# Kernel optimization log

Measured on AMD Instinct MI355X. Metric: run time of the kernel, lower is better.

Reference implementation:

```python
import jax, jax.numpy as jnp
import numpy as np

B, C, H, W = 4, 64, 64, 64
CQK = C // 8


def setup_inputs() -> dict:
    key = jax.random.key(0)
    k0, k1, k2, k3, k4 = jax.random.split(key, 5)
    x = jax.random.normal(k0, (B, C, H, W), dtype=jnp.float32)
    # Conv1d kernel_size=1, bias=False -> plain [out, in] matmul weights
    Wq = jax.random.normal(k1, (CQK, C), dtype=jnp.float32) * 0.05
    Wk = jax.random.normal(k2, (CQK, C), dtype=jnp.float32) * 0.05
    Wv = jax.random.normal(k3, (C, C), dtype=jnp.float32) * 0.05
    # torch init is 0; use a nonzero scalar so the attention path is exercised
    gamma = jax.random.uniform(k4, (1,), dtype=jnp.float32)
    return {"x": x, "Wq": Wq, "Wk": Wk, "Wv": Wv, "gamma": gamma}


def reference(x, Wq, Wk, Wv, gamma):
    shape = x.shape                      # [B, C, H, W]
    xf = x.reshape(shape[0], shape[1], -1)  # [B, C, N]
    q = jnp.einsum('oc,bcn->bon', Wq, xf)   # [B, C/8, N]
    k = jnp.einsum('oc,bcn->bon', Wk, xf)   # [B, C/8, N]
    v = jnp.einsum('oc,bcn->bon', Wv, xf)   # [B, C, N]
    # score[b, n, m] = sum_c q[b, c, n] * k[b, c, m]  (no 1/sqrt(d) scale)
    score = jnp.einsum('bcn,bcm->bnm', q, k)  # [B, N, N]
    # unconventional softmax over dim=1 (rows/first N axis, i.e. per-column)
    score = jax.nn.softmax(score, axis=1)
    out = jnp.einsum('bcn,bnm->bcm', v, score)  # [B, C, N]
    attention = gamma * out + xf
    return attention.reshape(shape)
```

## Files before the change

kernel.cpp:

```cpp
#include <hip/hip_runtime.h>

#define BB 4
#define NN 4096

typedef __attribute__((ext_vector_type(8))) short short8v;
typedef __attribute__((ext_vector_type(4))) short short4v;
typedef __attribute__((ext_vector_type(4))) float float4v;
typedef __attribute__((ext_vector_type(16))) float f32x16;

__device__ __forceinline__ unsigned short f2bf_rn(float f) {
    unsigned u = __float_as_uint(f);
    u += 0x7FFFu + ((u >> 16) & 1u);
    return (unsigned short)(u >> 16);
}

__global__ __launch_bounds__(256) void qkv_kernel(
    const float* __restrict__ x,
    const float* __restrict__ Wq, const float* __restrict__ Wk,
    const float* __restrict__ Wv,
    unsigned short* __restrict__ Qt, unsigned short* __restrict__ Kt,
    unsigned short* __restrict__ Vsw)
{
    __shared__ __align__(16) unsigned short xs[64][68];
    __shared__ __align__(16) unsigned short Ot[64][72];

    const int t    = threadIdx.x;
    const int w    = t >> 6;
    const int lane = t & 63;
    const int quad = lane >> 4;
    const int l15  = lane & 15;
    const int b    = blockIdx.y;
    const int n0   = blockIdx.x * 64;

    #pragma unroll
    for (int i = 0; i < 4; ++i) {
        int c  = (t >> 4) + i * 16;
        int n4 = (t & 15) * 4;
        float4 xv = *(const float4*)&x[(size_t)(b * 64 + c) * NN + n0 + n4];
        short4v pk;
        pk[0] = (short)f2bf_rn(xv.x); pk[1] = (short)f2bf_rn(xv.y);
        pk[2] = (short)f2bf_rn(xv.z); pk[3] = (short)f2bf_rn(xv.w);
        *(short4v*)&xs[c][n4] = pk;
    }

    short8v bw[5][2];
    #pragma unroll
    for (int ot = 0; ot < 5; ++ot) {
        int o = ot * 16 + l15;
        const float* base = (o < 8)  ? (Wq + o * 64)
                           : (o < 16) ? (Wk + (o - 8) * 64)
                                      : (Wv + (o - 16) * 64);
        const float scale = (o < 8) ? 1.4426950408889634f : 1.0f;
        #pragma unroll
        for (int h = 0; h < 2; ++h) {
            float4 u0 = *(const float4*)&base[h * 32 + quad * 8];
            float4 u1 = *(const float4*)&base[h * 32 + quad * 8 + 4];
            short8v f;
            f[0] = (short)f2bf_rn(u0.x * scale); f[1] = (short)f2bf_rn(u0.y * scale);
            f[2] = (short)f2bf_rn(u0.z * scale); f[3] = (short)f2bf_rn(u0.w * scale);
            f[4] = (short)f2bf_rn(u1.x * scale); f[5] = (short)f2bf_rn(u1.y * scale);
            f[6] = (short)f2bf_rn(u1.z * scale); f[7] = (short)f2bf_rn(u1.w * scale);
            bw[ot][h] = f;
        }
    }
    __syncthreads();

    short8v a0, a1;
    {
        unsigned short* p0 = (unsigned short*)&a0;
        unsigned short* p1 = (unsigned short*)&a1;
        const int nn = w * 16 + l15;
        #pragma unroll
        for (int j = 0; j < 8; ++j) {
            p0[j] = xs[quad * 8 + j][nn];
            p1[j] = xs[32 + quad * 8 + j][nn];
        }
    }

    const float4v zacc = {0.f, 0.f, 0.f, 0.f};
    #pragma unroll
    for (int ot = 0; ot < 5; ++ot) {
        float4v d = __builtin_amdgcn_mfma_f32_16x16x32_bf16(a0, bw[ot][0], zacc, 0, 0, 0);
        d = __builtin_amdgcn_mfma_f32_16x16x32_bf16(a1, bw[ot][1], d, 0, 0, 0);
        if (ot == 0) {
            #pragma unroll
            for (int r = 0; r < 4; ++r) {
                unsigned short v = f2bf_rn(d[r]);
                size_t n = (size_t)(n0 + w * 16 + quad * 4 + r);
                if (l15 < 8) Qt[((size_t)b * NN + n) * 8 + l15] = v;
                else         Kt[((size_t)b * NN + n) * 8 + (l15 - 8)] = v;
            }
        } else {
            short4v pk;
            #pragma unroll
            for (int r = 0; r < 4; ++r) pk[r] = (short)f2bf_rn(d[r]);
            *(short4v*)&Ot[(ot - 1) * 16 + l15][w * 16 + quad * 4] = pk;
        }
    }
    __syncthreads();

    #pragma unroll
    for (int h = 0; h < 2; ++h) {
        int ci  = w * 2 + h;
        int ct  = ci >> 2, nsl = ci & 3;
        short8v d = *(const short8v*)&Ot[ct * 32 + (lane & 31)][nsl * 16 + ((lane >> 5) << 3)];
        size_t ns = (size_t)blockIdx.x * 4 + nsl;
        unsigned short* cb = Vsw + (((size_t)b * 2 + ct) * 256 + ns) * 512;
        *(short8v*)(cb + lane * 8) = d;
    }
}

__global__ __launch_bounds__(512, 4) void attn_kernel(
    const unsigned short* __restrict__ Qt,
    const unsigned short* __restrict__ Kt,
    const unsigned short* __restrict__ Vsw,
    const float* __restrict__ x, const float* __restrict__ gamma,
    float* __restrict__ out)
{
    __shared__ __align__(16) float Ored[4][64][36];
    __shared__ __align__(16) float Lred[8][32];
    __shared__ __align__(16) float Lf[32];

    const int t    = threadIdx.x;
    const int w    = t >> 6;
    const int lane = t & 63;
    const int hi   = lane >> 5;
    const int l31  = lane & 31;
    const int b    = blockIdx.y;
    const int m0   = blockIdx.x * 32;

    const short8v zfrag = {0, 0, 0, 0, 0, 0, 0, 0};
    const f32x16 zero16 = {0.f, 0.f, 0.f, 0.f, 0.f, 0.f, 0.f, 0.f,
                           0.f, 0.f, 0.f, 0.f, 0.f, 0.f, 0.f, 0.f};

    short8v bk = zfrag;
    if (!hi) bk = *(const short8v*)(Kt + ((size_t)b * NN + m0 + l31) * 8);

    f32x16 acc0 = zero16, acc1 = zero16;
    float La = 0.f, Lb = 0.f;

    const unsigned short* qp  = Qt + ((size_t)b * NN + w * 512) * 8;
    const unsigned short* v0p = Vsw + ((size_t)b * 2 * 256 + w * 32) * 512 + lane * 8;
    const unsigned short* v1p = v0p + 256 * 512;

    short8v aqn = zfrag;
    if (!hi) aqn = *(const short8v*)(qp + (size_t)l31 * 8);

    for (int it = 0; it < 16; ++it) {
        short8v a00 = *(const short8v*)(v0p + it * 1024);
        short8v a01 = *(const short8v*)(v0p + it * 1024 + 512);
        short8v a10 = *(const short8v*)(v1p + it * 1024);
        short8v a11 = *(const short8v*)(v1p + it * 1024 + 512);

        short8v aq = aqn;

        f32x16 s = __builtin_amdgcn_mfma_f32_32x32x16_bf16(aq, bk, zero16, 0, 0, 0);

        const int itn = (it + 1) & 15;
        if (!hi) aqn = *(const short8v*)(qp + (size_t)(itn * 32 + l31) * 8);

        unsigned xw[8];
        #pragma unroll
        for (int j = 0; j < 8; ++j) {
            float e0 = __builtin_amdgcn_exp2f(s[2 * j]);
            float e1 = __builtin_amdgcn_exp2f(s[2 * j + 1]);
            La += e0;
            Lb += e1;
            asm("v_cvt_pk_bf16_f32 %0, %1, %2" : "=v"(xw[j]) : "v"(e0), "v"(e1));
        }

        asm("v_permlane32_swap_b32 %0, %1" : "+v"(xw[2]), "+v"(xw[0]));
        asm("v_permlane32_swap_b32 %0, %1" : "+v"(xw[3]), "+v"(xw[1]));
        asm("v_permlane32_swap_b32 %0, %1" : "+v"(xw[6]), "+v"(xw[4]));
        asm("v_permlane32_swap_b32 %0, %1" : "+v"(xw[7]), "+v"(xw[5]));

        union { unsigned u[4]; short8v v; } bp0, bp1;
        bp0.u[0] = xw[0]; bp0.u[1] = xw[1]; bp0.u[2] = xw[2]; bp0.u[3] = xw[3];
        bp1.u[0] = xw[4]; bp1.u[1] = xw[5]; bp1.u[2] = xw[6]; bp1.u[3] = xw[7];

        __builtin_amdgcn_s_setprio(1);
        acc0 = __builtin_amdgcn_mfma_f32_32x32x16_bf16(a00, bp0.v, acc0, 0, 0, 0);
        acc0 = __builtin_amdgcn_mfma_f32_32x32x16_bf16(a01, bp1.v, acc0, 0, 0, 0);
        acc1 = __builtin_amdgcn_mfma_f32_32x32x16_bf16(a10, bp0.v, acc1, 0, 0, 0);
        acc1 = __builtin_amdgcn_mfma_f32_32x32x16_bf16(a11, bp1.v, acc1, 0, 0, 0);
        __builtin_amdgcn_s_setprio(0);
    }

    float Lacc = La + Lb;

    Lacc += __shfl_xor(Lacc, 32, 64);
    if (lane < 32) Lred[w][l31] = Lacc;

    if (w < 4) {
        #pragma unroll
        for (int r = 0; r < 16; ++r) {
            int c = (r & 3) + 8 * (r >> 2) + 4 * hi;
            Ored[w][c][l31]      = acc0[r];
            Ored[w][c + 32][l31] = acc1[r];
        }
    }
    __syncthreads();
    if (w >= 4) {
        #pragma unroll
        for (int r = 0; r < 16; ++r) {
            int c = (r & 3) + 8 * (r >> 2) + 4 * hi;
            Ored[w - 4][c][l31]      += acc0[r];
            Ored[w - 4][c + 32][l31] += acc1[r];
        }
    }
    if (t < 32) {
        float sum = Lred[0][t] + Lred[1][t] + Lred[2][t] + Lred[3][t]
                  + Lred[4][t] + Lred[5][t] + Lred[6][t] + Lred[7][t];
        Lf[t] = 1.f / sum;
    }
    __syncthreads();

    {
        const float gv = gamma[0];
        int c = t >> 3, m4 = (t & 7) * 4;
        float4 o = {0.f, 0.f, 0.f, 0.f};
        #pragma unroll
        for (int k2 = 0; k2 < 4; ++k2) {
            float4 v = *(const float4*)&Ored[k2][c][m4];
            o.x += v.x; o.y += v.y; o.z += v.z; o.w += v.w;
        }
        float4 lf = *(const float4*)&Lf[m4];
        size_t gbase = ((size_t)b * 64 + c) * NN + m0 + m4;
        float4 xv = *(const float4*)&x[gbase];
        float4 r;
        r.x = gv * o.x * lf.x + xv.x;
        r.y = gv * o.y * lf.y + xv.y;
        r.z = gv * o.z * lf.z + xv.z;
        r.w = gv * o.w * lf.w + xv.w;
        *(float4*)&out[gbase] = r;
    }
}

extern "C" void kernel_launch(void* const* d_in, const int* in_sizes, int n_in,
                              void* d_out, int out_size, void* d_ws, size_t ws_size,
                              hipStream_t stream) {
    const float* x     = (const float*)d_in[0];
    const float* Wq    = (const float*)d_in[1];
    const float* Wk    = (const float*)d_in[2];
    const float* Wv    = (const float*)d_in[3];
    const float* gamma = (const float*)d_in[4];
    float* out = (float*)d_out;

    unsigned short* ws = (unsigned short*)d_ws;
    unsigned short* Qt  = ws;
    unsigned short* Kt  = Qt + (size_t)BB * NN * 8;
    unsigned short* Vsw = Kt + (size_t)BB * NN * 8;

    qkv_kernel<<<dim3(NN / 64, BB), 256, 0, stream>>>(x, Wq, Wk, Wv, Qt, Kt, Vsw);
    attn_kernel<<<dim3(NN / 32, BB), 512, 0, stream>>>(Qt, Kt, Vsw, x, gamma, out);
}
```

Baseline: 85.07 us.

## Split qkv projection into finer blocks and compute softmax denominators with MFMA

The projection kernel now handles 32 positions per block with 512 threads, so there are twice as many blocks and each wave computes only one or two output tiles instead of five. The attention kernel drops the per-element VALU accumulation of exponentials and instead gets the column sums from two extra MFMAs against an all-ones bf16 operand. This offloads adds from the VALU, which is already busy with exp and packing, to the matrix unit. The cost is extra MFMA work per iteration, and the denominators are now summed from bf16-rounded exponentials.

Result: no change. 85.80 us (+0.9%).

```diff
diff --git a/kernel.cpp b/kernel.cpp
--- a/kernel.cpp
+++ b/kernel.cpp
@@ -14,79 +14,85 @@
     return (unsigned short)(u >> 16);
 }
 
-__global__ __launch_bounds__(256) void qkv_kernel(
+__global__ __launch_bounds__(512) void qkv_kernel(
     const float* __restrict__ x,
     const float* __restrict__ Wq, const float* __restrict__ Wk,
     const float* __restrict__ Wv,
     unsigned short* __restrict__ Qt, unsigned short* __restrict__ Kt,
     unsigned short* __restrict__ Vsw)
 {
-    __shared__ __align__(16) unsigned short xs[64][68];
-    __shared__ __align__(16) unsigned short Ot[64][72];
+    __shared__ __align__(16) unsigned short xs[64][40];
+    __shared__ __align__(16) unsigned short Ot[64][40];
 
     const int t    = threadIdx.x;
     const int w    = t >> 6;
     const int lane = t & 63;
     const int quad = lane >> 4;
     const int l15  = lane & 15;
+    const int hi   = lane >> 5;
+    const int l31  = lane & 31;
     const int b    = blockIdx.y;
-    const int n0   = blockIdx.x * 64;
-
-    #pragma unroll
-    for (int i = 0; i < 4; ++i) {
-        int c  = (t >> 4) + i * 16;
-        int n4 = (t & 15) * 4;
+    const int n0   = blockIdx.x * 32;
+
+    const float4v zacc4 = {0.f, 0.f, 0.f, 0.f};
+
+    {
+        int c = t >> 3, n4 = (t & 7) * 4;
         float4 xv = *(const float4*)&x[(size_t)(b * 64 + c) * NN + n0 + n4];
         short4v pk;
         pk[0] = (short)f2bf_rn(xv.x); pk[1] = (short)f2bf_rn(xv.y);
         pk[2] = (short)f2bf_rn(xv.z); pk[3] = (short)f2bf_rn(xv.w);
         *(short4v*)&xs[c][n4] = pk;
     }
-
-    short8v bw[5][2];
+    __syncthreads();
+
     #pragma unroll
-    for (int ot = 0; ot < 5; ++ot) {
+    for (int ti = 0; ti < 2; ++ti) {
+        int ot, nt;
+        if (ti == 0) { ot = w >> 1; nt = w & 1; }
+        else         { if (w >= 2) break; ot = 4; nt = w; }
+
         int o = ot * 16 + l15;
         const float* base = (o < 8)  ? (Wq + o * 64)
                            : (o < 16) ? (Wk + (o - 8) * 64)
                                       : (Wv + (o - 16) * 64);
         const float scale = (o < 8) ? 1.4426950408889634f : 1.0f;
-        #pragma unroll
-        for (int h = 0; h < 2; ++h) {
-            float4 u0 = *(const float4*)&base[h * 32 + quad * 8];
-            float4 u1 = *(const float4*)&base[h * 32 + quad * 8 + 4];
-            short8v f;
-            f[0] = (short)f2bf_rn(u0.x * scale); f[1] = (short)f2bf_rn(u0.y * scale);
-            f[2] = (short)f2bf_rn(u0.z * scale); f[3] = (short)f2bf_rn(u0.w * scale);
-            f[4] = (short)f2bf_rn(u1.x * scale); f[5] = (short)f2bf_rn(u1.y * scale);
-            f[6] = (short)f2bf_rn(u1.z * scale); f[7] = (short)f2bf_rn(u1.w * scale);
-            bw[ot][h] = f;
-        }
-    }
-    __syncthreads();
-
-    short8v a0, a1;
-    {
-        unsigned short* p0 = (unsigned short*)&a0;
-        unsigned short* p1 = (unsigned short*)&a1;
-        const int nn = w * 16 + l15;
-        #pragma unroll
-        for (int j = 0; j < 8; ++j) {
-            p0[j] = xs[quad * 8 + j][nn];
-            p1[j] = xs[32 + quad * 8 + j][nn];
-        }
-    }
-
-    const float4v zacc = {0.f, 0.f, 0.f, 0.f};
-    #pragma unroll
-    for (int ot = 0; ot < 5; ++ot) {
-        float4v d = __builtin_amdgcn_mfma_f32_16x16x32_bf16(a0, bw[ot][0], zacc, 0, 0, 0);
-        d = __builtin_amdgcn_mfma_f32_16x16x32_bf16(a1, bw[ot][1], d, 0, 0, 0);
+        short8v bw0, bw1;
+        {
+            float4 u0 = *(const float4*)&base[quad * 8];
+            float4 u1 = *(const float4*)&base[quad * 8 + 4];
+            bw0[0] = (short)f2bf_rn(u0.x * scale); bw0[1] = (short)f2bf_rn(u0.y * scale);
+            bw0[2] = (short)f2bf_rn(u0.z * scale); bw0[3] = (short)f2bf_rn(u0.w * scale);
+            bw0[4] = (short)f2bf_rn(u1.x * scale); bw0[5] = (short)f2bf_rn(u1.y * scale);
+            bw0[6] = (short)f2bf_rn(u1.z * scale); bw0[7] = (short)f2bf_rn(u1.w * scale);
+            float4 u2 = *(const float4*)&base[32 + quad * 8];
+            float4 u3 = *(const float4*)&base[32 + quad * 8 + 4];
+            bw1[0] = (short)f2bf_rn(u2.x * scale); bw1[1] = (short)f2bf_rn(u2.y * scale);
+            bw1[2] = (short)f2bf_rn(u2.z * scale); bw1[3] = (short)f2bf_rn(u2.w * scale);
+            bw1[4] = (short)f2bf_rn(u3.x * scale); bw1[5] = (short)f2bf_rn(u3.y * scale);
+            bw1[6] = (short)f2bf_rn(u3.z * scale); bw1[7] = (short)f2bf_rn(u3.w * scale);
+        }
+
+        short8v a0, a1;
+        {
+            unsigned short* p0 = (unsigned short*)&a0;
+            unsigned short* p1 = (unsigned short*)&a1;
+            const int nn = nt * 16 + l15;
+            #pragma unroll
+            for (int j = 0; j < 8; ++j) {
+                p0[j] = xs[quad * 8 + j][nn];
+                p1[j] = xs[32 + quad * 8 + j][nn];
+            }
+        }
+
+        float4v d = __builtin_amdgcn_mfma_f32_16x16x32_bf16(a0, bw0, zacc4, 0, 0, 0);
+        d = __builtin_amdgcn_mfma_f32_16x16x32_bf16(a1, bw1, d, 0, 0, 0);
+
         if (ot == 0) {
             #pragma unroll
             for (int r = 0; r < 4; ++r) {
                 unsigned short v = f2bf_rn(d[r]);
-                size_t n = (size_t)(n0 + w * 16 + quad * 4 + r);
+                size_t n = (size_t)(n0 + nt * 16 + quad * 4 + r);
                 if (l15 < 8) Qt[((size_t)b * NN + n) * 8 + l15] = v;
                 else         Kt[((size_t)b * NN + n) * 8 + (l15 - 8)] = v;
             }
@@ -94,17 +100,15 @@
             short4v pk;
             #pragma unroll
             for (int r = 0; r < 4; ++r) pk[r] = (short)f2bf_rn(d[r]);
-            *(short4v*)&Ot[(ot - 1) * 16 + l15][w * 16 + quad * 4] = pk;
-        }
-    }
-    __syncthreads();
-
-    #pragma unroll
-    for (int h = 0; h < 2; ++h) {
-        int ci  = w * 2 + h;
-        int ct  = ci >> 2, nsl = ci & 3;
-        short8v d = *(const short8v*)&Ot[ct * 32 + (lane & 31)][nsl * 16 + ((lane >> 5) << 3)];
-        size_t ns = (size_t)blockIdx.x * 4 + nsl;
+            *(short4v*)&Ot[(ot - 1) * 16 + l15][nt * 16 + quad * 4] = pk;
+        }
+    }
+    __syncthreads();
+
+    if (w < 4) {
+        int ct = w >> 1, nsl = w & 1;
+        short8v d = *(const short8v*)&Ot[ct * 32 + l31][nsl * 16 + hi * 8];
+        size_t ns = (size_t)blockIdx.x * 2 + nsl;
         unsigned short* cb = Vsw + (((size_t)b * 2 + ct) * 256 + ns) * 512;
         *(short8v*)(cb + lane * 8) = d;
     }
@@ -130,14 +134,15 @@
     const int m0   = blockIdx.x * 32;
 
     const short8v zfrag = {0, 0, 0, 0, 0, 0, 0, 0};
+    const short8v aones = {16256, 16256, 16256, 16256,
+                           16256, 16256, 16256, 16256};
     const f32x16 zero16 = {0.f, 0.f, 0.f, 0.f, 0.f, 0.f, 0.f, 0.f,
                            0.f, 0.f, 0.f, 0.f, 0.f, 0.f, 0.f, 0.f};
 
     short8v bk = zfrag;
     if (!hi) bk = *(const short8v*)(Kt + ((size_t)b * NN + m0 + l31) * 8);
 
-    f32x16 acc0 = zero16, acc1 = zero16;
-    float La = 0.f, Lb = 0.f;
+    f32x16 acc0 = zero16, acc1 = zero16, accL = zero16;
 
     const unsigned short* qp  = Qt + ((size_t)b * NN + w * 512) * 8;
     const unsigned short* v0p = Vsw + ((size_t)b * 2 * 256 + w * 32) * 512 + lane * 8;
@@ -164,8 +169,6 @@
         for (int j = 0; j < 8; ++j) {
             float e0 = __builtin_amdgcn_exp2f(s[2 * j]);
             float e1 = __builtin_amdgcn_exp2f(s[2 * j + 1]);
-            La += e0;
-            Lb += e1;
             asm("v_cvt_pk_bf16_f32 %0, %1, %2" : "=v"(xw[j]) : "v"(e0), "v"(e1));
         }
 
@@ -183,13 +186,12 @@
         acc0 = __builtin_amdgcn_mfma_f32_32x32x16_bf16(a01, bp1.v, acc0, 0, 0, 0);
         acc1 = __builtin_amdgcn_mfma_f32_32x32x16_bf16(a10, bp0.v, acc1, 0, 0, 0);
         acc1 = __builtin_amdgcn_mfma_f32_32x32x16_bf16(a11, bp1.v, acc1, 0, 0, 0);
+        accL = __builtin_amdgcn_mfma_f32_32x32x16_bf16(aones, bp0.v, accL, 0, 0, 0);
+        accL = __builtin_amdgcn_mfma_f32_32x32x16_bf16(aones, bp1.v, accL, 0, 0, 0);
         __builtin_amdgcn_s_setprio(0);
     }
 
-    float Lacc = La + Lb;
-
-    Lacc += __shfl_xor(Lacc, 32, 64);
-    if (lane < 32) Lred[w][l31] = Lacc;
+    if (lane < 32) Lred[w][l31] = accL[0];
 
     if (w < 4) {
         #pragma unroll
@@ -251,6 +253,6 @@
     unsigned short* Kt  = Qt + (size_t)BB * NN * 8;
     unsigned short* Vsw = Kt + (size_t)BB * NN * 8;
 
-    qkv_kernel<<<dim3(NN / 64, BB), 256, 0, stream>>>(x, Wq, Wk, Wv, Qt, Kt, Vsw);
+    qkv_kernel<<<dim3(NN / 32, BB), 512, 0, stream>>>(x, Wq, Wk, Wv, Qt, Kt, Vsw);
     attn_kernel<<<dim3(NN / 32, BB), 512, 0, stream>>>(Qt, Kt, Vsw, x, gamma, out);
 }
```
